# Performance work log

Measured on AMD Instinct MI355X. Metric: run time of the kernel, lower is better.

Reference implementation:

```python
import jax, jax.numpy as jnp
import numpy as np


def _rel_dist(h, w, dtype):
    # cell-centered unit grid in [0,1], mapped to [-1,1]
    ys = (jnp.arange(h, dtype=dtype) + 0.5) / h
    xs = (jnp.arange(w, dtype=dtype) + 0.5) / w
    gy, gx = jnp.meshgrid(ys, xs, indexing='ij')     # (h, w)
    coords = 2.0 * jnp.stack([gy, gx], axis=-1) - 1.0  # (h, w, 2)
    c1 = coords[None, None, :, :, :]   # (1,1,h,w,2)  -> h2,w2
    c2 = coords[:, :, None, None, :]   # (h,w,1,1,2)  -> h1,w1
    return jnp.tanh(2.0 * (c1 - c2))   # (h1,w1,h2,w2,2)


def setup_inputs() -> dict:
    key = jax.random.key(0)
    ks = jax.random.split(key, 6)
    B, Ci, Co, H, W = 16, 16, 16, 24, 24
    hidden = 64
    v = jax.random.normal(ks[0], (B, Ci, H, W), dtype=jnp.float32)
    w1 = jax.random.normal(ks[1], (hidden, 2), dtype=jnp.float32) * (1.0 / np.sqrt(2.0))
    b1 = jax.random.normal(ks[2], (hidden,), dtype=jnp.float32) * 0.02
    w2 = jax.random.normal(ks[3], (Co * Ci, hidden), dtype=jnp.float32) * (1.0 / np.sqrt(hidden))
    b2 = jax.random.normal(ks[4], (Co * Ci,), dtype=jnp.float32) * 0.02
    bias = jax.random.normal(ks[5], (Co, 1, 1), dtype=jnp.float32) * (1.0 / np.sqrt(Ci))
    return {"v": v, "w1": w1, "b1": b1, "w2": w2, "b2": b2, "bias": bias}


def reference(v, w1, b1, w2, b2, bias):
    H, W = v.shape[-2], v.shape[-1]
    Co, Ci = bias.shape[0], v.shape[-3]
    rel = _rel_dist(H, W, v.dtype)                       # (h1,w1,h2,w2,2)
    hid = jax.nn.gelu(rel @ w1.T + b1, approximate=False)  # (h1,w1,h2,w2,64)
    kernel = (hid @ w2.T + b2).reshape(H, W, H, W, Co, Ci)  # (h1,w1,h2,w2,o,i)
    out = jnp.einsum('hwHWoi,biHW->bohw', kernel, v) / (H * W)
    return out + bias
```

## Files before the change

kernel.cpp:

```cpp
#include <hip/hip_runtime.h>
#include <hip/hip_bf16.h>


typedef __attribute__((ext_vector_type(8))) short bf16x8;
typedef __attribute__((ext_vector_type(4))) float f32x4;

#define KT_ELEMS (47*49*256)
#define VPAD2_ELEMS (40*40*256)
#define NROWS (47*49)
#define NPOS 576
#define NOCT 7
#define PREP_BUILD_BLOCKS 288
#define PREP_PAD_BLOCKS (VPAD2_ELEMS/256)

__launch_bounds__(256)
__global__ void prep(const float* __restrict__ v,
                     const float* __restrict__ w1, const float* __restrict__ b1,
                     const float* __restrict__ w2, const float* __restrict__ b2,
                     __hip_bfloat16* __restrict__ kt, __hip_bfloat16* __restrict__ vpad)
{
    const int tid = threadIdx.x;

    if (blockIdx.x >= PREP_BUILD_BLOCKS) {
        int idx = (blockIdx.x - PREP_BUILD_BLOCKS)*256 + tid;
        if (idx >= VPAD2_ELEMS) return;
        int i = idx & 15;
        int b = (idx >> 4) & 15;
        int s = idx >> 8;
        int x = s % 40;
        int y = s / 40;
        int h = y - 8, w = x - 8;
        float val = 0.0f;
        if (h >= 0 && h < 24 && w >= 0 && w < 24)
            val = v[((b*16 + i)*24 + h)*24 + w];
        vpad[idx] = __float2bfloat16(val);
        return;
    }

    __shared__ float ty_s[47];
    __shared__ float tx_s[49];
    __shared__ float hid_s[8][64];
    const int r0 = blockIdx.x * 8;

    if (tid < 47)               ty_s[tid]      = tanhf((float)(tid - 23) * (1.0f/6.0f));
    if (tid >= 64 && tid < 113) tx_s[tid - 64] = tanhf((float)(tid - 64 - 24) * (1.0f/6.0f));
    __syncthreads();

    #pragma unroll
    for (int k = 0; k < 2; ++k) {
        int idx = k*256 + tid;
        int rr  = idx >> 6;
        int j   = idx & 63;
        int r   = r0 + rr;
        if (r >= NROWS) r = NROWS - 1;
        int dy47 = r / 49;
        int dxi  = r % 49;
        float x = ty_s[dy47]*w1[2*j] + tx_s[dxi]*w1[2*j+1] + b1[j];
        hid_s[rr][j] = 0.5f*x*(1.0f + erff(x*0.70710678118f));
    }
    __syncthreads();

    const int c = tid;
    float acc[8];
    const float bb = b2[c];
    #pragma unroll
    for (int r = 0; r < 8; ++r) acc[r] = bb;

    const float4* w2v = (const float4*)w2;
    #pragma unroll
    for (int jv = 0; jv < 16; ++jv) {
        float4 wv = w2v[c*16 + jv];
        #pragma unroll
        for (int e = 0; e < 4; ++e) {
            float we = ((const float*)&wv)[e];
            int j = jv*4 + e;
            #pragma unroll
            for (int r = 0; r < 8; ++r)
                acc[r] += hid_s[r][j] * we;
        }
    }

    #pragma unroll
    for (int rr = 0; rr < 8; ++rr) {
        int r = r0 + rr;
        if (r >= NROWS) break;
        kt[r*256 + c] = __float2bfloat16(acc[rr]);
    }
}

__launch_bounds__(512)
__global__ void conv_part(const __hip_bfloat16* __restrict__ kt_,
                          const __hip_bfloat16* __restrict__ vpad_,
                          float* __restrict__ part)
{
    __shared__ f32x4 red[8][4][64];
    const short* kt = (const short*)kt_;
    const short* vp = (const short*)vpad_;

    const int wt  = blockIdx.x;
    const int hg  = blockIdx.y;
    const int oct = blockIdx.z;
    const int w0  = wt * 4;
    const int h0  = hg * 4;

    const int tid  = threadIdx.x;
    const int lane = tid & 63;
    const int wv   = tid >> 6;
    const int tq   = wv & 3;
    const int hhh  = wv >> 2;
    const int n    = lane & 15;
    const int g    = lane >> 4;
    const int d    = g >> 1;
    const int ih   = (g & 1) * 8;

    const int t = oct*4 + tq;

    f32x4 acc[2][4];
    #pragma unroll
    for (int hh = 0; hh < 2; ++hh)
        #pragma unroll
        for (int ww = 0; ww < 4; ++ww) acc[hh][ww] = (f32x4){0.f,0.f,0.f,0.f};

    if (t < 27) {
        const int dy47 = t - h0 + 20;
        const short* apb = kt + ((long)(dy47*49 + (24 - w0 + d)))*256 + n*16 + ih;
        const short* bpb = vp + ((long)((t + hhh*2 + 5)*40 + (8 + d)))*256 + n*16 + ih;

        bf16x8 av[4];
        av[0] = *(const bf16x8*)(apb);
        av[1] = *(const bf16x8*)(apb - 256);
        av[2] = *(const bf16x8*)(apb - 512);
        av[3] = *(const bf16x8*)(apb - 768);

        #pragma unroll
        for (int dxp = 0; dxp < 12; ++dxp) {
            bf16x8 bv0 = *(const bf16x8*)(bpb +         dxp*512);
            bf16x8 bv1 = *(const bf16x8*)(bpb + 10240 + dxp*512);
            #pragma unroll
            for (int ww = 0; ww < 4; ++ww) {
                acc[0][ww] = __builtin_amdgcn_mfma_f32_16x16x32_bf16(av[ww], bv0, acc[0][ww], 0, 0, 0);
                acc[1][ww] = __builtin_amdgcn_mfma_f32_16x16x32_bf16(av[ww], bv1, acc[1][ww], 0, 0, 0);
            }
            if (dxp < 11) {
                av[2] = av[0];
                av[3] = av[1];
                av[0] = *(const bf16x8*)(apb + (2*dxp + 2)*256);
                av[1] = *(const bf16x8*)(apb + (2*dxp + 1)*256);
            }
        }
    }

    #pragma unroll
    for (int hh = 0; hh < 2; ++hh) {
        if (hh) __syncthreads();
        #pragma unroll
        for (int ww = 0; ww < 4; ++ww) red[wv][ww][lane] = acc[hh][ww];
        __syncthreads();

        const int hhh2 = wv >> 2;
        const int ww2  = wv & 3;
        f32x4 s = red[0 + 0][ww2][lane];
        s = red[4*hhh2 + 0][ww2][lane];
        s += red[4*hhh2 + 1][ww2][lane];
        s += red[4*hhh2 + 2][ww2][lane];
        s += red[4*hhh2 + 3][ww2][lane];

        const int h = h0 + hhh2*2 + hh;
        const int w = w0 + ww2;
        const int p = h*24 + w;
        float* dst = part + ((size_t)oct*NPOS + p)*256 + (n*16 + g*4);
        *(f32x4*)dst = s;
    }
}

__launch_bounds__(256)
__global__ void combine(const float* __restrict__ part, const float* __restrict__ bias,
                        float* __restrict__ out)
{
    __shared__ float lds[16][257];
    const int tid = threadIdx.x;
    const int p0  = blockIdx.x * 16;

    #pragma unroll
    for (int pp = 0; pp < 16; ++pp) {
        float s = 0.f;
        #pragma unroll
        for (int oct = 0; oct < NOCT; ++oct)
            s += part[((size_t)oct*NPOS + p0 + pp)*256 + tid];
        lds[pp][tid] = s;
    }
    __syncthreads();

    const int pp = tid & 15;
    const int g  = tid >> 4;
    const float sc = 1.0f/576.0f;
    #pragma unroll
    for (int cc = 0; cc < 16; ++cc) {
        int c2 = cc*16 + g;
        out[(size_t)c2*576 + p0 + pp] = lds[pp][c2]*sc + bias[c2 & 15];
    }
}

extern "C" void kernel_launch(void* const* d_in, const int* in_sizes, int n_in,
                              void* d_out, int out_size, void* d_ws, size_t ws_size,
                              hipStream_t stream)
{
    const float* v    = (const float*)d_in[0];
    const float* w1   = (const float*)d_in[1];
    const float* b1   = (const float*)d_in[2];
    const float* w2   = (const float*)d_in[3];
    const float* b2   = (const float*)d_in[4];
    const float* bias = (const float*)d_in[5];
    float* out = (float*)d_out;

    char* ws = (char*)d_ws;
    __hip_bfloat16* kt   = (__hip_bfloat16*)ws;
    __hip_bfloat16* vpad = (__hip_bfloat16*)(ws + (size_t)KT_ELEMS*2);
    float* part = (float*)(ws + (size_t)KT_ELEMS*2 + (size_t)VPAD2_ELEMS*2);

    prep<<<dim3(PREP_BUILD_BLOCKS + PREP_PAD_BLOCKS), dim3(256), 0, stream>>>(
        v, w1, b1, w2, b2, kt, vpad);
    conv_part<<<dim3(6, 6, NOCT), dim3(512), 0, stream>>>(kt, vpad, part);
    combine<<<dim3(NPOS/16), dim3(256), 0, stream>>>(part, bias, out);
}
```

Measured before the change: 25.39 us.

## Replace partial-sum buffer and combine kernel with atomic accumulation into output

Removes the combine kernel and the partial-sum workspace. The prep kernel now also initializes the output with the bias, and conv_part atomically adds its scaled partial results straight into the output. This saves one kernel launch and the write and read of the partial buffer. In exchange it adds 7-way float atomics on the same addresses, scattered strided stores, and a summation order that is no longer deterministic.

New measurement: 78.21 us. 208% more time.

```diff
diff --git a/kernel.cpp b/kernel.cpp
--- a/kernel.cpp
+++ b/kernel.cpp
@@ -9,21 +9,31 @@
 #define VPAD2_ELEMS (40*40*256)
 #define NROWS (47*49)
 #define NPOS 576
+#define OUT_ELEMS (256*NPOS)
 #define NOCT 7
 #define PREP_BUILD_BLOCKS 288
 #define PREP_PAD_BLOCKS (VPAD2_ELEMS/256)
+#define PREP_OUT_BLOCKS (OUT_ELEMS/256)
 
 __launch_bounds__(256)
 __global__ void prep(const float* __restrict__ v,
                      const float* __restrict__ w1, const float* __restrict__ b1,
                      const float* __restrict__ w2, const float* __restrict__ b2,
-                     __hip_bfloat16* __restrict__ kt, __hip_bfloat16* __restrict__ vpad)
+                     const float* __restrict__ bias,
+                     __hip_bfloat16* __restrict__ kt, __hip_bfloat16* __restrict__ vpad,
+                     float* __restrict__ out)
 {
     const int tid = threadIdx.x;
-
-    if (blockIdx.x >= PREP_BUILD_BLOCKS) {
-        int idx = (blockIdx.x - PREP_BUILD_BLOCKS)*256 + tid;
-        if (idx >= VPAD2_ELEMS) return;
+    const int bid = blockIdx.x;
+
+    if (bid >= PREP_BUILD_BLOCKS + PREP_PAD_BLOCKS) {
+        int idx = (bid - PREP_BUILD_BLOCKS - PREP_PAD_BLOCKS)*256 + tid;
+        out[idx] = bias[(idx / NPOS) & 15];
+        return;
+    }
+
+    if (bid >= PREP_BUILD_BLOCKS) {
+        int idx = (bid - PREP_BUILD_BLOCKS)*256 + tid;
         int i = idx & 15;
         int b = (idx >> 4) & 15;
         int s = idx >> 8;
@@ -40,7 +50,7 @@
     __shared__ float ty_s[47];
     __shared__ float tx_s[49];
     __shared__ float hid_s[8][64];
-    const int r0 = blockIdx.x * 8;
+    const int r0 = bid * 8;
 
     if (tid < 47)               ty_s[tid]      = tanhf((float)(tid - 23) * (1.0f/6.0f));
     if (tid >= 64 && tid < 113) tx_s[tid - 64] = tanhf((float)(tid - 64 - 24) * (1.0f/6.0f));
@@ -91,7 +101,7 @@
 __launch_bounds__(512)
 __global__ void conv_part(const __hip_bfloat16* __restrict__ kt_,
                           const __hip_bfloat16* __restrict__ vpad_,
-                          float* __restrict__ part)
+                          float* __restrict__ out)
 {
     __shared__ f32x4 red[8][4][64];
     const short* kt = (const short*)kt_;
@@ -150,6 +160,7 @@
         }
     }
 
+    const float sc = 1.0f/576.0f;
     #pragma unroll
     for (int hh = 0; hh < 2; ++hh) {
         if (hh) __syncthreads();
@@ -159,8 +170,7 @@
 
         const int hhh2 = wv >> 2;
         const int ww2  = wv & 3;
-        f32x4 s = red[0 + 0][ww2][lane];
-        s = red[4*hhh2 + 0][ww2][lane];
+        f32x4 s = red[4*hhh2 + 0][ww2][lane];
         s += red[4*hhh2 + 1][ww2][lane];
         s += red[4*hhh2 + 2][ww2][lane];
         s += red[4*hhh2 + 3][ww2][lane];
@@ -168,36 +178,10 @@
         const int h = h0 + hhh2*2 + hh;
         const int w = w0 + ww2;
         const int p = h*24 + w;
-        float* dst = part + ((size_t)oct*NPOS + p)*256 + (n*16 + g*4);
-        *(f32x4*)dst = s;
-    }
-}
-
-__launch_bounds__(256)
-__global__ void combine(const float* __restrict__ part, const float* __restrict__ bias,
-                        float* __restrict__ out)
-{
-    __shared__ float lds[16][257];
-    const int tid = threadIdx.x;
-    const int p0  = blockIdx.x * 16;
-
-    #pragma unroll
-    for (int pp = 0; pp < 16; ++pp) {
-        float s = 0.f;
-        #pragma unroll
-        for (int oct = 0; oct < NOCT; ++oct)
-            s += part[((size_t)oct*NPOS + p0 + pp)*256 + tid];
-        lds[pp][tid] = s;
-    }
-    __syncthreads();
-
-    const int pp = tid & 15;
-    const int g  = tid >> 4;
-    const float sc = 1.0f/576.0f;
-    #pragma unroll
-    for (int cc = 0; cc < 16; ++cc) {
-        int c2 = cc*16 + g;
-        out[(size_t)c2*576 + p0 + pp] = lds[pp][c2]*sc + bias[c2 & 15];
+        float* dst = out + (size_t)(n*16 + g*4)*NPOS + p;
+        #pragma unroll
+        for (int e = 0; e < 4; ++e)
+            atomicAdd(dst + (size_t)e*NPOS, s[e]*sc);
     }
 }
 
@@ -216,10 +200,8 @@
     char* ws = (char*)d_ws;
     __hip_bfloat16* kt   = (__hip_bfloat16*)ws;
     __hip_bfloat16* vpad = (__hip_bfloat16*)(ws + (size_t)KT_ELEMS*2);
-    float* part = (float*)(ws + (size_t)KT_ELEMS*2 + (size_t)VPAD2_ELEMS*2);
-
-    prep<<<dim3(PREP_BUILD_BLOCKS + PREP_PAD_BLOCKS), dim3(256), 0, stream>>>(
-        v, w1, b1, w2, b2, kt, vpad);
-    conv_part<<<dim3(6, 6, NOCT), dim3(512), 0, stream>>>(kt, vpad, part);
-    combine<<<dim3(NPOS/16), dim3(256), 0, stream>>>(part, bias, out);
+
+    prep<<<dim3(PREP_BUILD_BLOCKS + PREP_PAD_BLOCKS + PREP_OUT_BLOCKS),
+           dim3(256), 0, stream>>>(v, w1, b1, w2, b2, bias, kt, vpad, out);
+    conv_part<<<dim3(6, 6, NOCT), dim3(512), 0, stream>>>(kt, vpad, out);
 }
```

## Fuse combine into conv kernel via last-block ticket reduction

Applied to the files above, without the earlier changes.

Removes the separate combine launch. Each conv block writes its partial, bumps an atomic ticket per spatial tile, and the last of the NOCT blocks for that tile sums the partials, scales, adds bias and writes output with float4 stores. This saves a kernel launch and its gap, at the cost of fences, an atomic per block and a serialized tail reduction in the last block. Tickets are reset in prep.

Measured after the change: 73.74 us. 2.9x slower.

```diff
diff --git a/kernel.cpp b/kernel.cpp
--- a/kernel.cpp
+++ b/kernel.cpp
@@ -17,7 +17,8 @@
 __global__ void prep(const float* __restrict__ v,
                      const float* __restrict__ w1, const float* __restrict__ b1,
                      const float* __restrict__ w2, const float* __restrict__ b2,
-                     __hip_bfloat16* __restrict__ kt, __hip_bfloat16* __restrict__ vpad)
+                     __hip_bfloat16* __restrict__ kt, __hip_bfloat16* __restrict__ vpad,
+                     int* __restrict__ tickets)
 {
     const int tid = threadIdx.x;
 
@@ -37,6 +38,8 @@
         return;
     }
 
+    if (blockIdx.x == 0 && tid < 36) tickets[tid] = 0;
+
     __shared__ float ty_s[47];
     __shared__ float tx_s[49];
     __shared__ float hid_s[8][64];
@@ -89,11 +92,15 @@
 }
 
 __launch_bounds__(512)
-__global__ void conv_part(const __hip_bfloat16* __restrict__ kt_,
-                          const __hip_bfloat16* __restrict__ vpad_,
-                          float* __restrict__ part)
+__global__ void conv_fused(const __hip_bfloat16* __restrict__ kt_,
+                           const __hip_bfloat16* __restrict__ vpad_,
+                           const float* __restrict__ bias,
+                           float* __restrict__ part,
+                           int* __restrict__ tickets,
+                           float* __restrict__ out)
 {
     __shared__ f32x4 red[8][4][64];
+    __shared__ int lastFlag;
     const short* kt = (const short*)kt_;
     const short* vp = (const short*)vpad_;
 
@@ -159,8 +166,7 @@
 
         const int hhh2 = wv >> 2;
         const int ww2  = wv & 3;
-        f32x4 s = red[0 + 0][ww2][lane];
-        s = red[4*hhh2 + 0][ww2][lane];
+        f32x4 s = red[4*hhh2 + 0][ww2][lane];
         s += red[4*hhh2 + 1][ww2][lane];
         s += red[4*hhh2 + 2][ww2][lane];
         s += red[4*hhh2 + 3][ww2][lane];
@@ -171,33 +177,46 @@
         float* dst = part + ((size_t)oct*NPOS + p)*256 + (n*16 + g*4);
         *(f32x4*)dst = s;
     }
-}
-
-__launch_bounds__(256)
-__global__ void combine(const float* __restrict__ part, const float* __restrict__ bias,
-                        float* __restrict__ out)
-{
-    __shared__ float lds[16][257];
-    const int tid = threadIdx.x;
-    const int p0  = blockIdx.x * 16;
-
-    #pragma unroll
-    for (int pp = 0; pp < 16; ++pp) {
+
+    __syncthreads();
+    __threadfence();
+    __syncthreads();
+    if (tid == 0) {
+        int tk = atomicAdd(&tickets[hg*6 + wt], 1);
+        lastFlag = (tk == NOCT - 1);
+    }
+    __syncthreads();
+    if (!lastFlag) return;
+    __threadfence();
+
+    float* sbuf = (float*)red;
+    const int c2 = tid & 255;
+    const int ph2 = tid >> 8;
+    #pragma unroll
+    for (int pl = 0; pl < 8; ++pl) {
+        int pos = ph2*8 + pl;
+        int p = (h0 + (pos >> 2))*24 + (w0 + (pos & 3));
         float s = 0.f;
         #pragma unroll
-        for (int oct = 0; oct < NOCT; ++oct)
-            s += part[((size_t)oct*NPOS + p0 + pp)*256 + tid];
-        lds[pp][tid] = s;
-    }
-    __syncthreads();
-
-    const int pp = tid & 15;
-    const int g  = tid >> 4;
+        for (int oc = 0; oc < NOCT; ++oc)
+            s += part[((size_t)oc*NPOS + p)*256 + c2];
+        sbuf[pos*256 + c2] = s;
+    }
+    __syncthreads();
+
     const float sc = 1.0f/576.0f;
     #pragma unroll
-    for (int cc = 0; cc < 16; ++cc) {
-        int c2 = cc*16 + g;
-        out[(size_t)c2*576 + p0 + pp] = lds[pp][c2]*sc + bias[c2 & 15];
+    for (int it = 0; it < 2; ++it) {
+        int q   = it*512 + tid;
+        int c2v = q & 255;
+        int hl  = q >> 8;
+        const float bb = bias[c2v & 15];
+        float4 o;
+        o.x = sbuf[(hl*4 + 0)*256 + c2v]*sc + bb;
+        o.y = sbuf[(hl*4 + 1)*256 + c2v]*sc + bb;
+        o.z = sbuf[(hl*4 + 2)*256 + c2v]*sc + bb;
+        o.w = sbuf[(hl*4 + 3)*256 + c2v]*sc + bb;
+        *(float4*)(out + (size_t)c2v*576 + (h0 + hl)*24 + w0) = o;
     }
 }
 
@@ -217,9 +236,11 @@
     __hip_bfloat16* kt   = (__hip_bfloat16*)ws;
     __hip_bfloat16* vpad = (__hip_bfloat16*)(ws + (size_t)KT_ELEMS*2);
     float* part = (float*)(ws + (size_t)KT_ELEMS*2 + (size_t)VPAD2_ELEMS*2);
+    int* tickets = (int*)(ws + (size_t)KT_ELEMS*2 + (size_t)VPAD2_ELEMS*2
+                             + (size_t)NOCT*NPOS*256*4);
 
     prep<<<dim3(PREP_BUILD_BLOCKS + PREP_PAD_BLOCKS), dim3(256), 0, stream>>>(
-        v, w1, b1, w2, b2, kt, vpad);
-    conv_part<<<dim3(6, 6, NOCT), dim3(512), 0, stream>>>(kt, vpad, part);
-    combine<<<dim3(NPOS/16), dim3(256), 0, stream>>>(part, bias, out);
+        v, w1, b1, w2, b2, kt, vpad, tickets);
+    conv_fused<<<dim3(6, 6, NOCT), dim3(512), 0, stream>>>(
+        kt, vpad, bias, part, tickets, out);
 }
```

## Split conv work along dx instead of output rows to double block count

Applied to the files above, without the earlier changes.

Each conv block now covers two output rows instead of four. The two half-blocks of waves split the 12-step dx loop into two 6-step halves instead of each taking different output rows, and the grid doubles to 6x12x7. An 8-way LDS reduction replaces the 4-way one, and only half the waves write partial sums. The aim is to raise parallelism and shorten each wave's serial MFMA chain, at the cost of more kt/vpad reloads per output and an extra reduction.

Measured after the change: 24.65 us. -2.9%, faster.

```diff
diff --git a/kernel.cpp b/kernel.cpp
--- a/kernel.cpp
+++ b/kernel.cpp
@@ -98,22 +98,22 @@
     const short* vp = (const short*)vpad_;
 
     const int wt  = blockIdx.x;
-    const int hg  = blockIdx.y;
+    const int hg2 = blockIdx.y;
     const int oct = blockIdx.z;
     const int w0  = wt * 4;
-    const int h0  = hg * 4;
+    const int h0  = hg2 * 2;
 
     const int tid  = threadIdx.x;
     const int lane = tid & 63;
     const int wv   = tid >> 6;
     const int tq   = wv & 3;
-    const int hhh  = wv >> 2;
+    const int dxh  = wv >> 2;
     const int n    = lane & 15;
     const int g    = lane >> 4;
     const int d    = g >> 1;
     const int ih   = (g & 1) * 8;
 
-    const int t = oct*4 + tq;
+    const int ts = oct*4 + tq;
 
     f32x4 acc[2][4];
     #pragma unroll
@@ -121,19 +121,21 @@
         #pragma unroll
         for (int ww = 0; ww < 4; ++ww) acc[hh][ww] = (f32x4){0.f,0.f,0.f,0.f};
 
-    if (t < 27) {
-        const int dy47 = t - h0 + 20;
+    if (ts < 25) {
+        const int dy47 = ts - h0 + 22;
         const short* apb = kt + ((long)(dy47*49 + (24 - w0 + d)))*256 + n*16 + ih;
-        const short* bpb = vp + ((long)((t + hhh*2 + 5)*40 + (8 + d)))*256 + n*16 + ih;
-
+        const short* bpb = vp + ((long)((ts + 7)*40 + (8 + d)))*256 + n*16 + ih;
+
+        const int dxp0 = dxh*6;
         bf16x8 av[4];
-        av[0] = *(const bf16x8*)(apb);
-        av[1] = *(const bf16x8*)(apb - 256);
-        av[2] = *(const bf16x8*)(apb - 512);
-        av[3] = *(const bf16x8*)(apb - 768);
-
-        #pragma unroll
-        for (int dxp = 0; dxp < 12; ++dxp) {
+        av[0] = *(const bf16x8*)(apb + (2*dxp0    )*256);
+        av[1] = *(const bf16x8*)(apb + (2*dxp0 - 1)*256);
+        av[2] = *(const bf16x8*)(apb + (2*dxp0 - 2)*256);
+        av[3] = *(const bf16x8*)(apb + (2*dxp0 - 3)*256);
+
+        #pragma unroll
+        for (int j = 0; j < 6; ++j) {
+            const int dxp = dxp0 + j;
             bf16x8 bv0 = *(const bf16x8*)(bpb +         dxp*512);
             bf16x8 bv1 = *(const bf16x8*)(bpb + 10240 + dxp*512);
             #pragma unroll
@@ -141,7 +143,7 @@
                 acc[0][ww] = __builtin_amdgcn_mfma_f32_16x16x32_bf16(av[ww], bv0, acc[0][ww], 0, 0, 0);
                 acc[1][ww] = __builtin_amdgcn_mfma_f32_16x16x32_bf16(av[ww], bv1, acc[1][ww], 0, 0, 0);
             }
-            if (dxp < 11) {
+            if (j < 5) {
                 av[2] = av[0];
                 av[3] = av[1];
                 av[0] = *(const bf16x8*)(apb + (2*dxp + 2)*256);
@@ -157,19 +159,17 @@
         for (int ww = 0; ww < 4; ++ww) red[wv][ww][lane] = acc[hh][ww];
         __syncthreads();
 
-        const int hhh2 = wv >> 2;
-        const int ww2  = wv & 3;
-        f32x4 s = red[0 + 0][ww2][lane];
-        s = red[4*hhh2 + 0][ww2][lane];
-        s += red[4*hhh2 + 1][ww2][lane];
-        s += red[4*hhh2 + 2][ww2][lane];
-        s += red[4*hhh2 + 3][ww2][lane];
-
-        const int h = h0 + hhh2*2 + hh;
-        const int w = w0 + ww2;
-        const int p = h*24 + w;
-        float* dst = part + ((size_t)oct*NPOS + p)*256 + (n*16 + g*4);
-        *(f32x4*)dst = s;
+        if (wv < 4) {
+            f32x4 s = red[0][wv][lane];
+            #pragma unroll
+            for (int src = 1; src < 8; ++src) s += red[src][wv][lane];
+
+            const int h = h0 + hh;
+            const int w = w0 + wv;
+            const int p = h*24 + w;
+            float* dst = part + ((size_t)oct*NPOS + p)*256 + (n*16 + g*4);
+            *(f32x4*)dst = s;
+        }
     }
 }
 
@@ -220,6 +220,6 @@
 
     prep<<<dim3(PREP_BUILD_BLOCKS + PREP_PAD_BLOCKS), dim3(256), 0, stream>>>(
         v, w1, b1, w2, b2, kt, vpad);
-    conv_part<<<dim3(6, 6, NOCT), dim3(512), 0, stream>>>(kt, vpad, part);
+    conv_part<<<dim3(6, 12, NOCT), dim3(512), 0, stream>>>(kt, vpad, part);
     combine<<<dim3(NPOS/16), dim3(256), 0, stream>>>(part, bias, out);
 }
```
